# Performance work log

Hardware: AMD Instinct MI355X
Metric: run time of the kernel (lower is better)

## Reference

```python
import jax, jax.numpy as jnp
import numpy as np

B, T, I, H, NC = 128, 512, 128, 512, 100


def setup_inputs() -> dict:
    key = jax.random.key(0)
    ks = jax.random.split(key, 16)
    x = jax.random.randint(ks[0], (B, T, 1), 0, NC + 1)
    # embedding table with padding row 0 zeroed (padding_idx=0)
    emb = (jax.random.normal(ks[1], (NC + 1, I)) * 1.0).at[0].set(0.0)
    # kaiming_normal_ fan_out, sigmoid nonlinearity -> std = 1/sqrt(fan_out)
    sx = 1.0 / np.sqrt(H)
    sc = 1.0 / np.sqrt(H)
    sp = 1.0 / np.sqrt(NC)
    return {
        "x": x,
        "emb": emb,
        "Wfx": jax.random.normal(ks[2], (I, H)) * sx,
        "Wfc": jax.random.normal(ks[3], (H, H)) * sc,
        "bf": jnp.zeros((H,)),
        "Wix": jax.random.normal(ks[4], (I, H)) * sx,
        "Wic": jax.random.normal(ks[5], (H, H)) * sc,
        "bi": jnp.zeros((H,)),
        "Wox": jax.random.normal(ks[6], (I, H)) * sx,
        "Woc": jax.random.normal(ks[7], (H, H)) * sc,
        "bo": jnp.zeros((H,)),
        "Wcx": jax.random.normal(ks[8], (I, H)) * sx,
        "bc": jnp.zeros((H,)),
        "Wph": jax.random.normal(ks[9], (H, NC)) * sp,
        "bp": jnp.zeros((NC,)),
    }


def reference(x, emb, Wfx, Wfc, bf, Wix, Wic, bi, Wox, Woc, bo, Wcx, bc, Wph, bp):
    idx = x[:, :, 0]                      # [B,T] int indices
    xe = emb[idx]                         # [B,T,I] embedded inputs
    h_dim = Wfc.shape[0]
    # Fuse the four input-side GEMMs into one, hoisted out of the recurrence.
    Wx = jnp.concatenate([Wfx, Wix, Wox, Wcx], axis=1)   # [I,4H]
    bx = jnp.concatenate([bf, bi, bo, bc])               # [4H]
    xg = jnp.einsum('bti,ih->bth', xe, Wx) + bx          # [B,T,4H]
    # Fuse the three peephole (cell-state) GEMMs into one per step.
    Wc = jnp.concatenate([Wfc, Wic, Woc], axis=1)        # [H,3H]
    reset = (idx > 0).astype(xg.dtype)                   # [B,T]

    def step(carry, inp):
        C, h = carry
        g, r = inp                        # g: [B,4H], r: [B]
        cg = C @ Wc                       # [B,3H]
        f = jax.nn.sigmoid(g[:, :h_dim] + cg[:, :h_dim])
        i = jax.nn.sigmoid(g[:, h_dim:2 * h_dim] + cg[:, h_dim:2 * h_dim])
        o = jax.nn.sigmoid(g[:, 2 * h_dim:3 * h_dim] + cg[:, 2 * h_dim:])
        c_tilde = jax.nn.sigmoid(g[:, 3 * h_dim:])        # note: sigmoid, not tanh (per source)
        Cn = (c_tilde * i + C * f) * r[:, None]           # reset on padding tokens
        hn = jnp.tanh(Cn) * o
        return (Cn, hn), None

    bsz = xg.shape[0]
    init = (jnp.zeros((bsz, h_dim), xg.dtype), jnp.zeros((bsz, h_dim), xg.dtype))
    xs = (jnp.swapaxes(xg, 0, 1), jnp.swapaxes(reset, 0, 1))  # time-major
    (Cf, hf), _ = jax.lax.scan(step, init, xs)
    p = hf @ Wph + bp                     # [B,num_classes]
    return jax.nn.log_softmax(p, axis=1)
```

## Files before the change

### kernel.cpp

```cpp
#include <hip/hip_runtime.h>
#include <hip/hip_bf16.h>
#include <stdint.h>

#define HD   512
#define ID   128
#define NCLS 100
#define TT   512
#define BB   128
#define NEMB 101
#define NGRP 32
#define GWG  8
#define RPG  4
#define COLS 64
#define THR  1024
#define CPAD 520
#define PST  5

#define WS_FLAG 0
#define WS_BAR  4096
#define WS_G    65536
#define WS_C0   (1u * 1024 * 1024)
#define WS_C1   (WS_C0 + 262144)
#define WS_HFB  (WS_C1 + 262144)
#define NBARU   4096

using bf16 = __hip_bfloat16;

__device__ __forceinline__ float b2f(bf16 v) { return __bfloat162float(v); }
__device__ __forceinline__ float sigf(float x) { return 1.0f / (1.0f + expf(-x)); }

__device__ __forceinline__ float cld(const float* p) {
    return __hip_atomic_load(p, __ATOMIC_RELAXED, __HIP_MEMORY_SCOPE_AGENT);
}
__device__ __forceinline__ void cst(float* p, float v) {
    __hip_atomic_store(p, v, __ATOMIC_RELAXED, __HIP_MEMORY_SCOPE_AGENT);
}

template <bool BF>
__device__ __forceinline__ float ldv(const void* p, int i) {
    if constexpr (BF) return b2f(((const bf16*)p)[i]);
    else              return ((const float*)p)[i];
}

__device__ __forceinline__ void gbarrier(unsigned* cnt, unsigned* iter) {
    __syncthreads();
    if (threadIdx.x == 0) {
        __hip_atomic_fetch_add(cnt, 1u, __ATOMIC_RELAXED, __HIP_MEMORY_SCOPE_AGENT);
        const unsigned tgt = (*iter + 1u) * GWG;
        while (__hip_atomic_load(cnt, __ATOMIC_RELAXED, __HIP_MEMORY_SCOPE_AGENT) < tgt)
            ;
    }
    ++*iter;
    __syncthreads();
}

__global__ void init_k(const uint32_t* __restrict__ emb_raw,
                       int* __restrict__ flag, unsigned* __restrict__ bars) {
    const int t = threadIdx.x;
    for (int k = t; k < NBARU; k += 1024) bars[k] = 0u;
    if (t == 0) {
        uint32_t acc = 0;
        for (int i = 64; i < 128; ++i) acc |= emb_raw[i];
        *flag = (acc == 0u) ? 0 : 1;
    }
}

template <bool BF>
__global__ void build_G(const int* __restrict__ flag,
                        const void* __restrict__ emb,
                        const void* __restrict__ Wfx, const void* __restrict__ Wix,
                        const void* __restrict__ Wox, const void* __restrict__ Wcx,
                        const void* __restrict__ bfv, const void* __restrict__ biv,
                        const void* __restrict__ bov, const void* __restrict__ bcv,
                        float* __restrict__ G) {
    if (*flag != (BF ? 1 : 0)) return;
    const int c   = blockIdx.x;
    const int j   = blockIdx.y * 256 + threadIdx.x;
    const int q   = j >> 9;
    const int col = j & 511;
    const void* W  = (q == 0) ? Wfx : (q == 1) ? Wix : (q == 2) ? Wox : Wcx;
    const void* bv = (q == 0) ? bfv : (q == 1) ? biv : (q == 2) ? bov : bcv;
    float acc = ldv<BF>(bv, col);
    for (int i = 0; i < ID; ++i)
        acc += ldv<BF>(emb, c * ID + i) * ldv<BF>(W, i * HD + col);
    if (q == 3) acc = sigf(acc);
    G[c * 2048 + j] = acc;
}

template <bool BF>
__global__ __launch_bounds__(THR, 1) void recur_bs(
    const int* __restrict__ flag, const int* __restrict__ x,
    const float* __restrict__ G,
    const void* __restrict__ Wfc, const void* __restrict__ Wic,
    const void* __restrict__ Woc,
    float* __restrict__ C0, float* __restrict__ C1,
    float* __restrict__ Hfb, unsigned* __restrict__ bars)
{
    if (*flag != (BF ? 1 : 0)) return;

    __shared__ __align__(16) float Cs[RPG * CPAD];
    __shared__ __align__(8)  float2 part2[2048 * PST];
    __shared__ int idx[RPG * TT];
    __shared__ int lz[RPG];

    const int blk   = blockIdx.x;
    const int grp   = blk >> 3;
    const int rank  = blk & 7;
    const int r0    = grp * RPG;
    const int h0    = rank * COLS;
    const int tid   = threadIdx.x;
    const int cp    = tid & 31;
    const int chunk = tid >> 5;
    unsigned* bar = bars + grp * 32;

    idx[tid]        = x[r0 * TT + tid];
    idx[tid + 1024] = x[r0 * TT + tid + 1024];
    if (tid < RPG) lz[tid] = -1;
    __syncthreads();
    if (tid < TT)
        #pragma unroll
        for (int r = 0; r < RPG; ++r)
            if (idx[r * TT + tid] == 0) atomicMax(&lz[r], tid);
    __syncthreads();
    int t0 = TT;
    #pragma unroll
    for (int r = 0; r < RPG; ++r) t0 = min(t0, lz[r] + 1);

    float wfA[16], wfB[16], wiA[16], wiB[16];
    #pragma unroll
    for (int k = 0; k < 16; ++k) {
        const int hp = chunk * 16 + k;
        wfA[k] = ldv<BF>(Wfc, hp * HD + h0 + cp);
        wfB[k] = ldv<BF>(Wfc, hp * HD + h0 + cp + 32);
        wiA[k] = ldv<BF>(Wic, hp * HD + h0 + cp);
        wiB[k] = ldv<BF>(Wic, hp * HD + h0 + cp + 32);
    }
    #pragma unroll
    for (int k = 0; k < 16; ++k)
        asm volatile("" : "+v"(wfA[k]), "+v"(wfB[k]), "+v"(wiA[k]), "+v"(wiB[k]));

    if (tid < COLS * RPG) {
        const int c = tid & 63, r = tid >> 6;
        cst(&C0[(r0 + r) * HD + h0 + c], 0.0f);
        cst(&C1[(r0 + r) * HD + h0 + c], 0.0f);
    }
    unsigned bi = 0;
    gbarrier(bar, &bi);

    float Creg = 0.0f;
    const int erow = tid >> 9;
    const int ehp  = tid & 511;
    const bool isUpd = (tid < COLS * RPG);
    const int uc = tid & 63, ur = tid >> 6;

    for (int t = t0; t < TT; ++t) {
        #pragma unroll
        for (int k = 0; k < 16; ++k)
            asm volatile("" : "+v"(wfA[k]), "+v"(wfB[k]), "+v"(wiA[k]), "+v"(wiB[k]));

        const float* cur = (t & 1) ? C1 : C0;
        float*       nxt = (t & 1) ? C0 : C1;

        float gf = 0.f, gi = 0.f, sgc = 0.f;
        int cl = 1;
        if (isUpd) {
            cl = idx[ur * TT + t];
            const float* Gr = G + cl * 2048;
            gf  = Gr[h0 + uc];
            gi  = Gr[512 + h0 + uc];
            sgc = Gr[1536 + h0 + uc];
        }

        {
            const float v0 = cld(cur + (r0 + erow) * HD + ehp);
            const float v1 = cld(cur + (r0 + erow + 2) * HD + ehp);
            Cs[erow * CPAD + ehp]       = v0;
            Cs[(erow + 2) * CPAD + ehp] = v1;
        }
        __syncthreads();

        float fA[RPG], fB[RPG], iA[RPG], iB[RPG];
        #pragma unroll
        for (int r = 0; r < RPG; ++r) { fA[r] = 0.f; fB[r] = 0.f; iA[r] = 0.f; iB[r] = 0.f; }
        {
            const int cb4 = chunk * 4;
            #pragma unroll
            for (int j = 0; j < 4; ++j) {
                const float a0 = wfA[4*j], a1 = wfA[4*j+1], a2 = wfA[4*j+2], a3 = wfA[4*j+3];
                const float b0 = wfB[4*j], b1 = wfB[4*j+1], b2 = wfB[4*j+2], b3 = wfB[4*j+3];
                const float c0 = wiA[4*j], c1 = wiA[4*j+1], c2 = wiA[4*j+2], c3 = wiA[4*j+3];
                const float d0 = wiB[4*j], d1 = wiB[4*j+1], d2 = wiB[4*j+2], d3 = wiB[4*j+3];
                #pragma unroll
                for (int r = 0; r < RPG; ++r) {
                    const float4 cv = reinterpret_cast<const float4*>(
                        Cs + r * CPAD)[cb4 + j];
                    fA[r] += a0*cv.x + a1*cv.y + a2*cv.z + a3*cv.w;
                    fB[r] += b0*cv.x + b1*cv.y + b2*cv.z + b3*cv.w;
                    iA[r] += c0*cv.x + c1*cv.y + c2*cv.z + c3*cv.w;
                    iB[r] += d0*cv.x + d1*cv.y + d2*cv.z + d3*cv.w;
                }
            }
        }
        {
            float2* ppA = part2 + (chunk * 64 + cp)      * PST;
            float2* ppB = part2 + (chunk * 64 + cp + 32) * PST;
            #pragma unroll
            for (int r = 0; r < RPG; ++r) {
                ppA[r] = make_float2(fA[r], iA[r]);
                ppB[r] = make_float2(fB[r], iB[r]);
            }
        }
        __syncthreads();

        if (isUpd) {
            float df = 0.f, di = 0.f;
            #pragma unroll
            for (int ch = 0; ch < 32; ++ch) {
                const float2 v = part2[(ch * 64 + uc) * PST + ur];
                df += v.x;
                di += v.y;
            }
            float Cn = sgc * sigf(gi + di) + Creg * sigf(gf + df);
            Cn = (cl > 0) ? Cn : 0.0f;
            Creg = Cn;
            cst(&nxt[(r0 + ur) * HD + h0 + uc], Cn);
        }
        gbarrier(bar, &bi);
    }

    {
        const float v0 = cld(C1 + (r0 + erow) * HD + ehp);
        const float v1 = cld(C1 + (r0 + erow + 2) * HD + ehp);
        Cs[erow * CPAD + ehp]       = v0;
        Cs[(erow + 2) * CPAD + ehp] = v1;
        __syncthreads();

        const int oc = tid & 63, och = tid >> 6;
        float ao[RPG];
        #pragma unroll
        for (int r = 0; r < RPG; ++r) ao[r] = 0.0f;
        #pragma unroll 4
        for (int k = 0; k < 32; ++k) {
            const int hp = och * 32 + k;
            const float wo = ldv<BF>(Woc, hp * HD + h0 + oc);
            #pragma unroll
            for (int r = 0; r < RPG; ++r)
                ao[r] += wo * Cs[r * CPAD + hp];
        }
        {
            float2* pp = part2 + (och * 64 + oc) * PST;
            #pragma unroll
            for (int r2 = 0; r2 < RPG / 2; ++r2)
                pp[r2] = make_float2(ao[2 * r2], ao[2 * r2 + 1]);
        }
        __syncthreads();
        if (isUpd) {
            float s = 0.f;
            #pragma unroll
            for (int ch = 0; ch < 16; ++ch) {
                const float2 v = part2[(ch * 64 + uc) * PST + (ur >> 1)];
                s += (ur & 1) ? v.y : v.x;
            }
            const int cl2 = idx[ur * TT + TT - 1];
            const float o = sigf(G[cl2 * 2048 + 1024 + h0 + uc] + s);
            Hfb[(r0 + ur) * HD + h0 + uc] = tanhf(Creg) * o;
        }
    }
}

template <bool BF>
__global__ __launch_bounds__(128) void proj(
    const int* __restrict__ flag, const float* __restrict__ Hfb,
    const void* __restrict__ Wph, const void* __restrict__ bp,
    void* __restrict__ out)
{
    if (*flag != (BF ? 1 : 0)) return;
    __shared__ __align__(16) float hv[HD];
    __shared__ float p_s[NCLS];
    __shared__ float lse_s;
    const int b   = blockIdx.x;
    const int tid = threadIdx.x;

    reinterpret_cast<float4*>(hv)[tid] =
        reinterpret_cast<const float4*>(Hfb + b * HD)[tid];
    __syncthreads();

    if (tid < NCLS) {
        float p = ldv<BF>(bp, tid);
        for (int h = 0; h < HD; ++h)
            p += hv[h] * ldv<BF>(Wph, h * NCLS + tid);
        p_s[tid] = p;
    }
    __syncthreads();
    if (tid == 0) {
        float m = -1e30f;
        for (int n = 0; n < NCLS; ++n) m = fmaxf(m, p_s[n]);
        float sum = 0.0f;
        for (int n = 0; n < NCLS; ++n) sum += expf(p_s[n] - m);
        lse_s = m + logf(sum);
    }
    __syncthreads();
    if (tid < NCLS) {
        const float v = p_s[tid] - lse_s;
        if constexpr (BF) ((bf16*)out)[b * NCLS + tid] = __float2bfloat16(v);
        else              ((float*)out)[b * NCLS + tid] = v;
    }
}

extern "C" void kernel_launch(void* const* d_in, const int* in_sizes, int n_in,
                              void* d_out, int out_size, void* d_ws, size_t ws_size,
                              hipStream_t stream) {
    const int*  x   = (const int*)d_in[0];
    const void* emb = d_in[1];
    const void* Wfx = d_in[2];
    const void* Wfc = d_in[3];
    const void* bfv = d_in[4];
    const void* Wix = d_in[5];
    const void* Wic = d_in[6];
    const void* biv = d_in[7];
    const void* Wox = d_in[8];
    const void* Woc = d_in[9];
    const void* bov = d_in[10];
    const void* Wcx = d_in[11];
    const void* bcv = d_in[12];
    const void* Wph = d_in[13];
    const void* bp  = d_in[14];

    int*      flag = (int*)((char*)d_ws + WS_FLAG);
    unsigned* bars = (unsigned*)((char*)d_ws + WS_BAR);
    float*    G    = (float*)((char*)d_ws + WS_G);
    float*    C0   = (float*)((char*)d_ws + WS_C0);
    float*    C1   = (float*)((char*)d_ws + WS_C1);
    float*    Hfb  = (float*)((char*)d_ws + WS_HFB);

    init_k<<<1, 1024, 0, stream>>>((const uint32_t*)emb, flag, bars);

    build_G<false><<<dim3(NEMB, 8), 256, 0, stream>>>(flag, emb, Wfx, Wix, Wox, Wcx,
                                                      bfv, biv, bov, bcv, G);
    build_G<true ><<<dim3(NEMB, 8), 256, 0, stream>>>(flag, emb, Wfx, Wix, Wox, Wcx,
                                                      bfv, biv, bov, bcv, G);

    {
        void* args[] = {(void*)&flag, (void*)&x, (void*)&G,
                        (void*)&Wfc, (void*)&Wic, (void*)&Woc,
                        (void*)&C0, (void*)&C1, (void*)&Hfb, (void*)&bars};
        hipLaunchCooperativeKernel((const void*)recur_bs<false>, dim3(NGRP * GWG), dim3(THR),
                                   args, 0, stream);
        hipLaunchCooperativeKernel((const void*)recur_bs<true>, dim3(NGRP * GWG), dim3(THR),
                                   args, 0, stream);
    }

    proj<false><<<BB, 128, 0, stream>>>(flag, Hfb, Wph, bp, d_out);
    proj<true ><<<BB, 128, 0, stream>>>(flag, Hfb, Wph, bp, d_out);
}
```

Baseline: 1.655 ms.

## Replace group atomic barrier with per-peer step flags and direct C exchange

Each block in a batch group now publishes its slice of the new cell state, writes it into its own shared copy, and raises a per-row step flag. Dedicated idle waves poll the flags of each peer and copy that peer's slice into shared memory. This replaces the counter-based group barrier and the full reload of the cell state from global memory at every timestep. It depends on relaxed atomics plus an explicit vmcnt wait for ordering, which may be fragile across the two double-buffered arrays. It also uses a larger flag area.

```diff
diff --git a/kernel.cpp b/kernel.cpp
--- a/kernel.cpp
+++ b/kernel.cpp
@@ -22,7 +22,7 @@
 #define WS_C0   (1u * 1024 * 1024)
 #define WS_C1   (WS_C0 + 262144)
 #define WS_HFB  (WS_C1 + 262144)
-#define NBARU   4096
+#define NBARU   8192
 
 using bf16 = __hip_bfloat16;
 
@@ -33,6 +33,12 @@
     return __hip_atomic_load(p, __ATOMIC_RELAXED, __HIP_MEMORY_SCOPE_AGENT);
 }
 __device__ __forceinline__ void cst(float* p, float v) {
+    __hip_atomic_store(p, v, __ATOMIC_RELAXED, __HIP_MEMORY_SCOPE_AGENT);
+}
+__device__ __forceinline__ unsigned cldu(const unsigned* p) {
+    return __hip_atomic_load(p, __ATOMIC_RELAXED, __HIP_MEMORY_SCOPE_AGENT);
+}
+__device__ __forceinline__ void cstu(unsigned* p, unsigned v) {
     __hip_atomic_store(p, v, __ATOMIC_RELAXED, __HIP_MEMORY_SCOPE_AGENT);
 }
 
@@ -40,18 +46,6 @@
 __device__ __forceinline__ float ldv(const void* p, int i) {
     if constexpr (BF) return b2f(((const bf16*)p)[i]);
     else              return ((const float*)p)[i];
-}
-
-__device__ __forceinline__ void gbarrier(unsigned* cnt, unsigned* iter) {
-    __syncthreads();
-    if (threadIdx.x == 0) {
-        __hip_atomic_fetch_add(cnt, 1u, __ATOMIC_RELAXED, __HIP_MEMORY_SCOPE_AGENT);
-        const unsigned tgt = (*iter + 1u) * GWG;
-        while (__hip_atomic_load(cnt, __ATOMIC_RELAXED, __HIP_MEMORY_SCOPE_AGENT) < tgt)
-            ;
-    }
-    ++*iter;
-    __syncthreads();
 }
 
 __global__ void init_k(const uint32_t* __restrict__ emb_raw,
@@ -94,7 +88,7 @@
     const void* __restrict__ Wfc, const void* __restrict__ Wic,
     const void* __restrict__ Woc,
     float* __restrict__ C0, float* __restrict__ C1,
-    float* __restrict__ Hfb, unsigned* __restrict__ bars)
+    float* __restrict__ Hfb, unsigned* __restrict__ flags)
 {
     if (*flag != (BF ? 1 : 0)) return;
 
@@ -111,10 +105,13 @@
     const int tid   = threadIdx.x;
     const int cp    = tid & 31;
     const int chunk = tid >> 5;
-    unsigned* bar = bars + grp * 32;
+    const int sw    = tid >> 6;
+    const int sl    = tid & 63;
+    unsigned* myf = flags + (grp * 8 + rank) * 32;
 
     idx[tid]        = x[r0 * TT + tid];
     idx[tid + 1024] = x[r0 * TT + tid + 1024];
+    for (int k = tid; k < RPG * CPAD; k += THR) Cs[k] = 0.0f;
     if (tid < RPG) lz[tid] = -1;
     __syncthreads();
     if (tid < TT)
@@ -139,17 +136,7 @@
     for (int k = 0; k < 16; ++k)
         asm volatile("" : "+v"(wfA[k]), "+v"(wfB[k]), "+v"(wiA[k]), "+v"(wiB[k]));
 
-    if (tid < COLS * RPG) {
-        const int c = tid & 63, r = tid >> 6;
-        cst(&C0[(r0 + r) * HD + h0 + c], 0.0f);
-        cst(&C1[(r0 + r) * HD + h0 + c], 0.0f);
-    }
-    unsigned bi = 0;
-    gbarrier(bar, &bi);
-
     float Creg = 0.0f;
-    const int erow = tid >> 9;
-    const int ehp  = tid & 511;
     const bool isUpd = (tid < COLS * RPG);
     const int uc = tid & 63, ur = tid >> 6;
 
@@ -158,8 +145,8 @@
         for (int k = 0; k < 16; ++k)
             asm volatile("" : "+v"(wfA[k]), "+v"(wfB[k]), "+v"(wiA[k]), "+v"(wiB[k]));
 
-        const float* cur = (t & 1) ? C1 : C0;
-        float*       nxt = (t & 1) ? C0 : C1;
+        float* pub = (t & 1) ? C1 : C0;
+        const bool lastStep = (t == TT - 1);
 
         float gf = 0.f, gi = 0.f, sgc = 0.f;
         int cl = 1;
@@ -170,14 +157,6 @@
             gi  = Gr[512 + h0 + uc];
             sgc = Gr[1536 + h0 + uc];
         }
-
-        {
-            const float v0 = cld(cur + (r0 + erow) * HD + ehp);
-            const float v1 = cld(cur + (r0 + erow + 2) * HD + ehp);
-            Cs[erow * CPAD + ehp]       = v0;
-            Cs[(erow + 2) * CPAD + ehp] = v1;
-        }
-        __syncthreads();
 
         float fA[RPG], fB[RPG], iA[RPG], iB[RPG];
         #pragma unroll
@@ -223,18 +202,38 @@
             float Cn = sgc * sigf(gi + di) + Creg * sigf(gf + df);
             Cn = (cl > 0) ? Cn : 0.0f;
             Creg = Cn;
-            cst(&nxt[(r0 + ur) * HD + h0 + uc], Cn);
-        }
-        gbarrier(bar, &bi);
+            if (!lastStep) {
+                cst(&pub[(r0 + ur) * HD + h0 + uc], Cn);
+                Cs[ur * CPAD + h0 + uc] = Cn;
+                asm volatile("s_waitcnt vmcnt(0)" ::: "memory");
+                if (uc == 0) cstu(&myf[ur], (unsigned)(t + 1));
+            }
+        } else if (sw >= 8 && !lastStep) {
+            const int q = sw - 8;
+            if (q != rank) {
+                const unsigned* qf = flags + (grp * 8 + q) * 32;
+                const unsigned tq = (unsigned)(t + 1);
+                for (;;) {
+                    const unsigned a = cldu(qf + 0), b = cldu(qf + 1);
+                    const unsigned c = cldu(qf + 2), d = cldu(qf + 3);
+                    if (a >= tq && b >= tq && c >= tq && d >= tq) break;
+                }
+                asm volatile("" ::: "memory");
+                const float* src = pub + r0 * HD + q * COLS + sl;
+                const float v0 = cld(src);
+                const float v1 = cld(src + HD);
+                const float v2 = cld(src + 2 * HD);
+                const float v3 = cld(src + 3 * HD);
+                Cs[0 * CPAD + q * COLS + sl] = v0;
+                Cs[1 * CPAD + q * COLS + sl] = v1;
+                Cs[2 * CPAD + q * COLS + sl] = v2;
+                Cs[3 * CPAD + q * COLS + sl] = v3;
+            }
+        }
+        __syncthreads();
     }
 
     {
-        const float v0 = cld(C1 + (r0 + erow) * HD + ehp);
-        const float v1 = cld(C1 + (r0 + erow + 2) * HD + ehp);
-        Cs[erow * CPAD + ehp]       = v0;
-        Cs[(erow + 2) * CPAD + ehp] = v1;
-        __syncthreads();
-
         const int oc = tid & 63, och = tid >> 6;
         float ao[RPG];
         #pragma unroll
@@ -326,14 +325,14 @@
     const void* Wph = d_in[13];
     const void* bp  = d_in[14];
 
-    int*      flag = (int*)((char*)d_ws + WS_FLAG);
-    unsigned* bars = (unsigned*)((char*)d_ws + WS_BAR);
-    float*    G    = (float*)((char*)d_ws + WS_G);
-    float*    C0   = (float*)((char*)d_ws + WS_C0);
-    float*    C1   = (float*)((char*)d_ws + WS_C1);
-    float*    Hfb  = (float*)((char*)d_ws + WS_HFB);
-
-    init_k<<<1, 1024, 0, stream>>>((const uint32_t*)emb, flag, bars);
+    int*      flag  = (int*)((char*)d_ws + WS_FLAG);
+    unsigned* flags = (unsigned*)((char*)d_ws + WS_BAR);
+    float*    G     = (float*)((char*)d_ws + WS_G);
+    float*    C0    = (float*)((char*)d_ws + WS_C0);
+    float*    C1    = (float*)((char*)d_ws + WS_C1);
+    float*    Hfb   = (float*)((char*)d_ws + WS_HFB);
+
+    init_k<<<1, 1024, 0, stream>>>((const uint32_t*)emb, flag, flags);
 
     build_G<false><<<dim3(NEMB, 8), 256, 0, stream>>>(flag, emb, Wfx, Wix, Wox, Wcx,
                                                       bfv, biv, bov, bcv, G);
@@ -343,7 +342,7 @@
     {
         void* args[] = {(void*)&flag, (void*)&x, (void*)&G,
                         (void*)&Wfc, (void*)&Wic, (void*)&Woc,
-                        (void*)&C0, (void*)&C1, (void*)&Hfb, (void*)&bars};
+                        (void*)&C0, (void*)&C1, (void*)&Hfb, (void*)&flags};
         hipLaunchCooperativeKernel((const void*)recur_bs<false>, dim3(NGRP * GWG), dim3(THR),
                                    args, 0, stream);
         hipLaunchCooperativeKernel((const void*)recur_bs<true>, dim3(NGRP * GWG), dim3(THR),
```

Result: slower. 2.142 ms (+29.4%).

## Halve recurrence block to 512 threads with 64 weights per thread and padded C layout

Applied to the files above, without the earlier changes.

Shrinks the recurrent block from 1024 to 512 threads. Each thread now holds four column strips of the Wfc/Wic slices in registers (128 floats) instead of two. The shared cell-state buffer gets a padded layout (20 floats per 16 elements) to cut LDS bank conflicts on the float4 reads, and the launch-bounds hint allows two blocks per CU. The intent is fewer threads per block barrier and more compute per LDS load, at the cost of higher register pressure that could cause spills.

```diff
diff --git a/kernel.cpp b/kernel.cpp
--- a/kernel.cpp
+++ b/kernel.cpp
@@ -12,8 +12,8 @@
 #define GWG  8
 #define RPG  4
 #define COLS 64
-#define THR  1024
-#define CPAD 520
+#define THR  512
+#define CPAD 640
 #define PST  5
 
 #define WS_FLAG 0
@@ -41,6 +41,8 @@
     if constexpr (BF) return b2f(((const bf16*)p)[i]);
     else              return ((const float*)p)[i];
 }
+
+__device__ __forceinline__ int cpi(int h) { return (h >> 4) * 20 + (h & 15); }
 
 __device__ __forceinline__ void gbarrier(unsigned* cnt, unsigned* iter) {
     __syncthreads();
@@ -88,7 +90,7 @@
 }
 
 template <bool BF>
-__global__ __launch_bounds__(THR, 1) void recur_bs(
+__global__ __launch_bounds__(THR, 2) void recur_bs(
     const int* __restrict__ flag, const int* __restrict__ x,
     const float* __restrict__ G,
     const void* __restrict__ Wfc, const void* __restrict__ Wic,
@@ -109,35 +111,42 @@
     const int r0    = grp * RPG;
     const int h0    = rank * COLS;
     const int tid   = threadIdx.x;
-    const int cp    = tid & 31;
-    const int chunk = tid >> 5;
+    const int cp    = tid & 15;
+    const int chunk = tid >> 4;
     unsigned* bar = bars + grp * 32;
 
     idx[tid]        = x[r0 * TT + tid];
+    idx[tid + 512]  = x[r0 * TT + tid + 512];
     idx[tid + 1024] = x[r0 * TT + tid + 1024];
+    idx[tid + 1536] = x[r0 * TT + tid + 1536];
     if (tid < RPG) lz[tid] = -1;
     __syncthreads();
-    if (tid < TT)
-        #pragma unroll
-        for (int r = 0; r < RPG; ++r)
-            if (idx[r * TT + tid] == 0) atomicMax(&lz[r], tid);
+    #pragma unroll
+    for (int r = 0; r < RPG; ++r)
+        if (idx[r * TT + tid] == 0) atomicMax(&lz[r], tid);
     __syncthreads();
     int t0 = TT;
     #pragma unroll
     for (int r = 0; r < RPG; ++r) t0 = min(t0, lz[r] + 1);
 
-    float wfA[16], wfB[16], wiA[16], wiB[16];
+    float wf0[16], wf1[16], wf2[16], wf3[16];
+    float wi0[16], wi1[16], wi2[16], wi3[16];
     #pragma unroll
     for (int k = 0; k < 16; ++k) {
         const int hp = chunk * 16 + k;
-        wfA[k] = ldv<BF>(Wfc, hp * HD + h0 + cp);
-        wfB[k] = ldv<BF>(Wfc, hp * HD + h0 + cp + 32);
-        wiA[k] = ldv<BF>(Wic, hp * HD + h0 + cp);
-        wiB[k] = ldv<BF>(Wic, hp * HD + h0 + cp + 32);
+        wf0[k] = ldv<BF>(Wfc, hp * HD + h0 + cp);
+        wf1[k] = ldv<BF>(Wfc, hp * HD + h0 + cp + 16);
+        wf2[k] = ldv<BF>(Wfc, hp * HD + h0 + cp + 32);
+        wf3[k] = ldv<BF>(Wfc, hp * HD + h0 + cp + 48);
+        wi0[k] = ldv<BF>(Wic, hp * HD + h0 + cp);
+        wi1[k] = ldv<BF>(Wic, hp * HD + h0 + cp + 16);
+        wi2[k] = ldv<BF>(Wic, hp * HD + h0 + cp + 32);
+        wi3[k] = ldv<BF>(Wic, hp * HD + h0 + cp + 48);
     }
     #pragma unroll
     for (int k = 0; k < 16; ++k)
-        asm volatile("" : "+v"(wfA[k]), "+v"(wfB[k]), "+v"(wiA[k]), "+v"(wiB[k]));
+        asm volatile("" : "+v"(wf0[k]), "+v"(wf1[k]), "+v"(wf2[k]), "+v"(wf3[k]),
+                          "+v"(wi0[k]), "+v"(wi1[k]), "+v"(wi2[k]), "+v"(wi3[k]));
 
     if (tid < COLS * RPG) {
         const int c = tid & 63, r = tid >> 6;
@@ -148,15 +157,15 @@
     gbarrier(bar, &bi);
 
     float Creg = 0.0f;
-    const int erow = tid >> 9;
-    const int ehp  = tid & 511;
     const bool isUpd = (tid < COLS * RPG);
     const int uc = tid & 63, ur = tid >> 6;
+    const int pe = cpi(tid);
 
     for (int t = t0; t < TT; ++t) {
         #pragma unroll
         for (int k = 0; k < 16; ++k)
-            asm volatile("" : "+v"(wfA[k]), "+v"(wfB[k]), "+v"(wiA[k]), "+v"(wiB[k]));
+            asm volatile("" : "+v"(wf0[k]), "+v"(wf1[k]), "+v"(wf2[k]), "+v"(wf3[k]),
+                              "+v"(wi0[k]), "+v"(wi1[k]), "+v"(wi2[k]), "+v"(wi3[k]));
 
         const float* cur = (t & 1) ? C1 : C0;
         float*       nxt = (t & 1) ? C0 : C1;
@@ -172,42 +181,54 @@
         }
 
         {
-            const float v0 = cld(cur + (r0 + erow) * HD + ehp);
-            const float v1 = cld(cur + (r0 + erow + 2) * HD + ehp);
-            Cs[erow * CPAD + ehp]       = v0;
-            Cs[(erow + 2) * CPAD + ehp] = v1;
+            const float v0 = cld(cur + (r0 + 0) * HD + tid);
+            const float v1 = cld(cur + (r0 + 1) * HD + tid);
+            const float v2 = cld(cur + (r0 + 2) * HD + tid);
+            const float v3 = cld(cur + (r0 + 3) * HD + tid);
+            Cs[0 * CPAD + pe] = v0;
+            Cs[1 * CPAD + pe] = v1;
+            Cs[2 * CPAD + pe] = v2;
+            Cs[3 * CPAD + pe] = v3;
         }
         __syncthreads();
 
-        float fA[RPG], fB[RPG], iA[RPG], iB[RPG];
+        float f0[RPG], f1[RPG], f2[RPG], f3[RPG];
+        float i0[RPG], i1[RPG], i2[RPG], i3[RPG];
         #pragma unroll
-        for (int r = 0; r < RPG; ++r) { fA[r] = 0.f; fB[r] = 0.f; iA[r] = 0.f; iB[r] = 0.f; }
+        for (int r = 0; r < RPG; ++r) {
+            f0[r] = 0.f; f1[r] = 0.f; f2[r] = 0.f; f3[r] = 0.f;
+            i0[r] = 0.f; i1[r] = 0.f; i2[r] = 0.f; i3[r] = 0.f;
+        }
         {
-            const int cb4 = chunk * 4;
+            const int cb = chunk * 5;
             #pragma unroll
             for (int j = 0; j < 4; ++j) {
-                const float a0 = wfA[4*j], a1 = wfA[4*j+1], a2 = wfA[4*j+2], a3 = wfA[4*j+3];
-                const float b0 = wfB[4*j], b1 = wfB[4*j+1], b2 = wfB[4*j+2], b3 = wfB[4*j+3];
-                const float c0 = wiA[4*j], c1 = wiA[4*j+1], c2 = wiA[4*j+2], c3 = wiA[4*j+3];
-                const float d0 = wiB[4*j], d1 = wiB[4*j+1], d2 = wiB[4*j+2], d3 = wiB[4*j+3];
                 #pragma unroll
                 for (int r = 0; r < RPG; ++r) {
                     const float4 cv = reinterpret_cast<const float4*>(
-                        Cs + r * CPAD)[cb4 + j];
-                    fA[r] += a0*cv.x + a1*cv.y + a2*cv.z + a3*cv.w;
-                    fB[r] += b0*cv.x + b1*cv.y + b2*cv.z + b3*cv.w;
-                    iA[r] += c0*cv.x + c1*cv.y + c2*cv.z + c3*cv.w;
-                    iB[r] += d0*cv.x + d1*cv.y + d2*cv.z + d3*cv.w;
+                        Cs + r * CPAD)[cb + j];
+                    f0[r] += wf0[4*j]*cv.x + wf0[4*j+1]*cv.y + wf0[4*j+2]*cv.z + wf0[4*j+3]*cv.w;
+                    f1[r] += wf1[4*j]*cv.x + wf1[4*j+1]*cv.y + wf1[4*j+2]*cv.z + wf1[4*j+3]*cv.w;
+                    f2[r] += wf2[4*j]*cv.x + wf2[4*j+1]*cv.y + wf2[4*j+2]*cv.z + wf2[4*j+3]*cv.w;
+                    f3[r] += wf3[4*j]*cv.x + wf3[4*j+1]*cv.y + wf3[4*j+2]*cv.z + wf3[4*j+3]*cv.w;
+                    i0[r] += wi0[4*j]*cv.x + wi0[4*j+1]*cv.y + wi0[4*j+2]*cv.z + wi0[4*j+3]*cv.w;
+                    i1[r] += wi1[4*j]*cv.x + wi1[4*j+1]*cv.y + wi1[4*j+2]*cv.z + wi1[4*j+3]*cv.w;
+                    i2[r] += wi2[4*j]*cv.x + wi2[4*j+1]*cv.y + wi2[4*j+2]*cv.z + wi2[4*j+3]*cv.w;
+                    i3[r] += wi3[4*j]*cv.x + wi3[4*j+1]*cv.y + wi3[4*j+2]*cv.z + wi3[4*j+3]*cv.w;
                 }
             }
         }
         {
-            float2* ppA = part2 + (chunk * 64 + cp)      * PST;
-            float2* ppB = part2 + (chunk * 64 + cp + 32) * PST;
+            float2* p0 = part2 + (chunk * 64 + cp)      * PST;
+            float2* p1 = part2 + (chunk * 64 + cp + 16) * PST;
+            float2* p2 = part2 + (chunk * 64 + cp + 32) * PST;
+            float2* p3 = part2 + (chunk * 64 + cp + 48) * PST;
             #pragma unroll
             for (int r = 0; r < RPG; ++r) {
-                ppA[r] = make_float2(fA[r], iA[r]);
-                ppB[r] = make_float2(fB[r], iB[r]);
+                p0[r] = make_float2(f0[r], i0[r]);
+                p1[r] = make_float2(f1[r], i1[r]);
+                p2[r] = make_float2(f2[r], i2[r]);
+                p3[r] = make_float2(f3[r], i3[r]);
             }
         }
         __syncthreads();
@@ -229,10 +250,14 @@
     }
 
     {
-        const float v0 = cld(C1 + (r0 + erow) * HD + ehp);
-        const float v1 = cld(C1 + (r0 + erow + 2) * HD + ehp);
-        Cs[erow * CPAD + ehp]       = v0;
-        Cs[(erow + 2) * CPAD + ehp] = v1;
+        const float v0 = cld(C1 + (r0 + 0) * HD + tid);
+        const float v1 = cld(C1 + (r0 + 1) * HD + tid);
+        const float v2 = cld(C1 + (r0 + 2) * HD + tid);
+        const float v3 = cld(C1 + (r0 + 3) * HD + tid);
+        Cs[0 * CPAD + pe] = v0;
+        Cs[1 * CPAD + pe] = v1;
+        Cs[2 * CPAD + pe] = v2;
+        Cs[3 * CPAD + pe] = v3;
         __syncthreads();
 
         const int oc = tid & 63, och = tid >> 6;
@@ -240,12 +265,13 @@
         #pragma unroll
         for (int r = 0; r < RPG; ++r) ao[r] = 0.0f;
         #pragma unroll 4
-        for (int k = 0; k < 32; ++k) {
-            const int hp = och * 32 + k;
+        for (int k = 0; k < 64; ++k) {
+            const int hp = och * 64 + k;
+            const int hpp = cpi(hp);
             const float wo = ldv<BF>(Woc, hp * HD + h0 + oc);
             #pragma unroll
             for (int r = 0; r < RPG; ++r)
-                ao[r] += wo * Cs[r * CPAD + hp];
+                ao[r] += wo * Cs[r * CPAD + hpp];
         }
         {
             float2* pp = part2 + (och * 64 + oc) * PST;
@@ -257,7 +283,7 @@
         if (isUpd) {
             float s = 0.f;
             #pragma unroll
-            for (int ch = 0; ch < 16; ++ch) {
+            for (int ch = 0; ch < 8; ++ch) {
                 const float2 v = part2[(ch * 64 + uc) * PST + (ur >> 1)];
                 s += (ur & 1) ? v.y : v.x;
             }
```

Result: faster. 1.605 ms (-3.1%).
